# Kernel optimization log

Measured on AMD Instinct MI355X. Metric: run time of the kernel, lower is better.

The kernel has to match this reference:

```python
import jax, jax.numpy as jnp
import numpy as np

B, S, D, H, HD = 1, 4096, 1024, 16, 64
ROPE_THETA = 10000.0


def setup_inputs() -> dict:
    key = jax.random.key(0)
    ks = jax.random.split(key, 10)
    sc = 0.02
    hidden_states = jax.random.normal(ks[0], (B, S, D), dtype=jnp.float32)
    # sorted continuous timestamps in [0, S) (irregularly sampled time series)
    timestamps = jnp.sort(jax.random.uniform(ks[1], (B, S), dtype=jnp.float32), axis=-1) * S
    Wq = jax.random.normal(ks[2], (D, D), dtype=jnp.float32) * sc
    bq = jax.random.normal(ks[3], (D,), dtype=jnp.float32) * sc
    Wk = jax.random.normal(ks[4], (D, D), dtype=jnp.float32) * sc
    bk = jax.random.normal(ks[5], (D,), dtype=jnp.float32) * sc
    Wv = jax.random.normal(ks[6], (D, D), dtype=jnp.float32) * sc
    bv = jax.random.normal(ks[7], (D,), dtype=jnp.float32) * sc
    Wo = jax.random.normal(ks[8], (D, D), dtype=jnp.float32) * sc
    return dict(hidden_states=hidden_states, timestamps=timestamps,
                Wq=Wq, bq=bq, Wk=Wk, bk=bk, Wv=Wv, bv=bv, Wo=Wo)


def _rotate_half(x):
    x1, x2 = jnp.split(x, 2, axis=-1)
    return jnp.concatenate([-x2, x1], axis=-1)


def _ct_rope(q, k, timestamps):
    # q,k: [b,h,s,hd]; timestamps: [b,s] continuous positions
    inv_freq = 1.0 / (ROPE_THETA ** (jnp.arange(0, HD, 2, dtype=jnp.float32) / HD))
    angles = timestamps[:, None, :, None] * inv_freq  # [b,1,s,hd/2]
    angles = jnp.concatenate([angles, angles], axis=-1)  # [b,1,s,hd]
    cos, sin = jnp.cos(angles), jnp.sin(angles)
    q = q * cos + _rotate_half(q) * sin
    k = k * cos + _rotate_half(k) * sin
    return q, k


def reference(hidden_states, timestamps, Wq, bq, Wk, bk, Wv, bv, Wo):
    b, s, _ = hidden_states.shape
    # nn.Linear convention: y = x @ W.T + b
    q = (hidden_states @ Wq.T + bq).reshape(b, s, H, HD).transpose(0, 2, 1, 3)
    k = (hidden_states @ Wk.T + bk).reshape(b, s, H, HD).transpose(0, 2, 1, 3)
    v = (hidden_states @ Wv.T + bv).reshape(b, s, H, HD).transpose(0, 2, 1, 3)
    q, k = _ct_rope(q, k, timestamps)
    scores = jnp.einsum('bhqd,bhkd->bhqk', q, k) / jnp.sqrt(jnp.float32(HD))
    # causal additive mask (built as in HF Qwen2Model)
    causal = jnp.tril(jnp.ones((s, s), dtype=bool))
    neg = jnp.finfo(jnp.float32).min
    scores = jnp.where(causal[None, None], scores, neg)
    attn = jax.nn.softmax(scores.astype(jnp.float32), axis=-1).astype(q.dtype)
    out = jnp.einsum('bhqk,bhkd->bhqd', attn, v)
    out = out.transpose(0, 2, 1, 3).reshape(b, s, H * HD)
    return out @ Wo.T
```

## Files before the change

kernel.cpp:

```cpp
#include <hip/hip_runtime.h>

#define S_LEN  4096
#define DMODEL 1024
#define NHEAD  16
#define HDIM   64

typedef float    f32x4  __attribute__((ext_vector_type(4)));
typedef float    f32x16 __attribute__((ext_vector_type(16)));
typedef _Float16 f16x8  __attribute__((ext_vector_type(8)));
typedef _Float16 f16x4v __attribute__((ext_vector_type(4)));
typedef __fp16   fp16x2 __attribute__((ext_vector_type(2)));
typedef unsigned int u32;
typedef u32 u32x4 __attribute__((ext_vector_type(4)));

__device__ __forceinline__ void gl2lds16(const _Float16* g, _Float16* l) {
  __builtin_amdgcn_global_load_lds(
      (const __attribute__((address_space(1))) unsigned int*)g,
      (__attribute__((address_space(3))) unsigned int*)l, 16, 0, 0);
}

__device__ __forceinline__ u32 pkrtz_u(float a, float b) {
  fp16x2 h = __builtin_amdgcn_cvt_pkrtz(a, b);
  return __builtin_bit_cast(u32, h);
}

__device__ __forceinline__ float m3(float a, float b, float c) {
  return fmaxf(fmaxf(a, b), c);
}

__global__ void cast_f32_f16_k(const float* __restrict__ in,
                               _Float16* __restrict__ out, int n) {
  int i = (blockIdx.x * blockDim.x + threadIdx.x) * 4;
  if (i + 3 < n) {
    const float4 v = *(const float4*)(in + i);
    f16x4v o = { (_Float16)v.x, (_Float16)v.y, (_Float16)v.z, (_Float16)v.w };
    *(f16x4v*)(out + i) = o;
  }
}

__global__ void cast4_k(const float* __restrict__ a, const float* __restrict__ b,
                        const float* __restrict__ c, const float* __restrict__ d,
                        _Float16* __restrict__ oa, _Float16* __restrict__ ob,
                        _Float16* __restrict__ oc, _Float16* __restrict__ od) {
  const int seg = blockIdx.y;
  const float* in = seg == 0 ? a : seg == 1 ? b : seg == 2 ? c : d;
  _Float16*   out = seg == 0 ? oa : seg == 1 ? ob : seg == 2 ? oc : od;
  const int i = (blockIdx.x * blockDim.x + threadIdx.x) * 4;
  const float4 v = *(const float4*)(in + i);
  f16x4v o = { (_Float16)v.x, (_Float16)v.y, (_Float16)v.z, (_Float16)v.w };
  *(f16x4v*)(out + i) = o;
}

__global__ __launch_bounds__(256)
void gemm_qkv(const _Float16* __restrict__ A,
              const _Float16* __restrict__ Bw,
              const float* __restrict__ bq,
              const float* __restrict__ bk,
              const float* __restrict__ bv,
              const float* __restrict__ ts,
              _Float16* __restrict__ Qb,
              _Float16* __restrict__ Kb,
              _Float16* __restrict__ Vtb)
{
  __shared__ _Float16 lA[128 * 64];
  __shared__ _Float16 lB[128 * 64];

  const int tid  = threadIdx.x;
  const int wid  = tid >> 6;
  const int lane = tid & 63;
  const int l16  = lane & 15;
  const int lg   = lane >> 4;
  const int wr = wid >> 1, wc = wid & 1;
  const int m0 = blockIdx.y * 128, n0 = blockIdx.x * 128;
  const int K = DMODEL, M = S_LEN;

  const int lrow   = lane >> 3;
  const int gchunk = (lane & 7) ^ lrow;

  f32x4 acc[4][4] = {};

  for (int k0 = 0; k0 < K; k0 += 64) {
#pragma unroll
    for (int it = 0; it < 4; ++it) {
      const int rbase = (it * 4 + wid) * 8;
      gl2lds16(A  + (size_t)(m0 + rbase + lrow) * K + k0 + gchunk * 8, &lA[rbase * 64]);
      gl2lds16(Bw + (size_t)(n0 + rbase + lrow) * K + k0 + gchunk * 8, &lB[rbase * 64]);
    }
    __syncthreads();
#pragma unroll
    for (int kk = 0; kk < 2; ++kk) {
      f16x8 af[4], bfr[4];
#pragma unroll
      for (int mr = 0; mr < 4; ++mr) {
        const int row = wr * 64 + mr * 16 + l16;
        const int ch  = (kk * 4 + lg) ^ (l16 & 7);
        af[mr] = *(const f16x8*)&lA[row * 64 + ch * 8];
      }
#pragma unroll
      for (int nr = 0; nr < 4; ++nr) {
        const int row = wc * 64 + nr * 16 + l16;
        const int ch  = (kk * 4 + lg) ^ (l16 & 7);
        bfr[nr] = *(const f16x8*)&lB[row * 64 + ch * 8];
      }
#pragma unroll
      for (int mr = 0; mr < 4; ++mr)
#pragma unroll
        for (int nr = 0; nr < 4; ++nr)
          acc[mr][nr] = __builtin_amdgcn_mfma_f32_16x16x32_f16(af[mr], bfr[nr], acc[mr][nr], 0, 0, 0);
    }
    __syncthreads();
  }

  if (n0 >= 2048) {
    const int dbase = n0 - 2048;
    float bvv[4];
#pragma unroll
    for (int nr = 0; nr < 4; ++nr) bvv[nr] = bv[dbase + wc * 64 + nr * 16 + l16];
#pragma unroll
    for (int mr = 0; mr < 4; ++mr) {
      const int mbase = m0 + wr * 64 + mr * 16 + lg * 4;
#pragma unroll
      for (int nr = 0; nr < 4; ++nr) {
        const int d = dbase + wc * 64 + nr * 16 + l16;
        f16x4v o = { (_Float16)(acc[mr][nr][0] + bvv[nr]),
                     (_Float16)(acc[mr][nr][1] + bvv[nr]),
                     (_Float16)(acc[mr][nr][2] + bvv[nr]),
                     (_Float16)(acc[mr][nr][3] + bvv[nr]) };
        *(f16x4v*)&Vtb[(size_t)d * M + mbase] = o;
      }
    }
  } else {
    _Float16* O = (n0 < 1024) ? Qb : Kb;
    const float* bias = (n0 < 1024) ? bq : bk;
    const int nloc = n0 & 1023;
    float bvv[4];
#pragma unroll
    for (int nr = 0; nr < 4; ++nr) bvv[nr] = bias[nloc + wc * 64 + nr * 16 + l16];
    const float L2T  = 13.287712379549449f / 32.0f;
    const float inv0 = exp2f(-(float)l16 * L2T);
    const float inv1 = exp2f(-(float)(l16 + 16) * L2T);
#pragma unroll
    for (int mr = 0; mr < 4; ++mr)
#pragma unroll
      for (int r = 0; r < 4; ++r) {
        const int m = m0 + wr * 64 + mr * 16 + lg * 4 + r;
        const float t = ts[m];
        float s0, c0, s1, c1;
        sincosf(t * inv0, &s0, &c0);
        sincosf(t * inv1, &s1, &c1);
        const float p0 = acc[mr][0][r] + bvv[0];
        const float p1 = acc[mr][1][r] + bvv[1];
        const float p2 = acc[mr][2][r] + bvv[2];
        const float p3 = acc[mr][3][r] + bvv[3];
        const size_t base = (size_t)m * DMODEL + nloc + wc * 64 + l16;
        O[base + 0 ] = (_Float16)(p0 * c0 - p2 * s0);
        O[base + 16] = (_Float16)(p1 * c1 - p3 * s1);
        O[base + 32] = (_Float16)(p2 * c0 + p0 * s0);
        O[base + 48] = (_Float16)(p3 * c1 + p1 * s1);
      }
  }
}

__global__ __launch_bounds__(256)
void gemm_o(const _Float16* __restrict__ A,
            const _Float16* __restrict__ Bw,
            float* __restrict__ O)
{
  __shared__ _Float16 lA[128 * 64];
  __shared__ _Float16 lB[128 * 64];

  const int tid  = threadIdx.x;
  const int wid  = tid >> 6;
  const int lane = tid & 63;
  const int l16  = lane & 15;
  const int lg   = lane >> 4;
  const int wr = wid >> 1, wc = wid & 1;
  const int m0 = blockIdx.y * 128, n0 = blockIdx.x * 128;
  const int K = DMODEL, N = DMODEL;

  const int lrow   = lane >> 3;
  const int gchunk = (lane & 7) ^ lrow;

  f32x4 acc[4][4] = {};

  for (int k0 = 0; k0 < K; k0 += 64) {
#pragma unroll
    for (int it = 0; it < 4; ++it) {
      const int rbase = (it * 4 + wid) * 8;
      gl2lds16(A  + (size_t)(m0 + rbase + lrow) * K + k0 + gchunk * 8, &lA[rbase * 64]);
      gl2lds16(Bw + (size_t)(n0 + rbase + lrow) * K + k0 + gchunk * 8, &lB[rbase * 64]);
    }
    __syncthreads();
#pragma unroll
    for (int kk = 0; kk < 2; ++kk) {
      f16x8 af[4], bfr[4];
#pragma unroll
      for (int mr = 0; mr < 4; ++mr) {
        const int row = wr * 64 + mr * 16 + l16;
        const int ch  = (kk * 4 + lg) ^ (l16 & 7);
        af[mr] = *(const f16x8*)&lA[row * 64 + ch * 8];
      }
#pragma unroll
      for (int nr = 0; nr < 4; ++nr) {
        const int row = wc * 64 + nr * 16 + l16;
        const int ch  = (kk * 4 + lg) ^ (l16 & 7);
        bfr[nr] = *(const f16x8*)&lB[row * 64 + ch * 8];
      }
#pragma unroll
      for (int mr = 0; mr < 4; ++mr)
#pragma unroll
        for (int nr = 0; nr < 4; ++nr)
          acc[mr][nr] = __builtin_amdgcn_mfma_f32_16x16x32_f16(af[mr], bfr[nr], acc[mr][nr], 0, 0, 0);
    }
    __syncthreads();
  }

#pragma unroll
  for (int mr = 0; mr < 4; ++mr)
#pragma unroll
    for (int r = 0; r < 4; ++r) {
      const int m = m0 + wr * 64 + mr * 16 + lg * 4 + r;
#pragma unroll
      for (int nr = 0; nr < 4; ++nr) {
        const int n = n0 + wc * 64 + nr * 16 + l16;
        O[(size_t)m * N + n] = acc[mr][nr][r];
      }
    }
}

__device__ __forceinline__ void stage_tiles(const _Float16* __restrict__ Km,
                                            const _Float16* __restrict__ Vt,
                                            _Float16* kdst, _Float16* vdst,
                                            int kv0, int h, int wid, int lane) {
#pragma unroll
  for (int j8 = 0; j8 < 2; ++j8) {
    const int rb  = wid * 16 + j8 * 8;
    const int row = rb + (lane >> 3);
    const int g   = (lane & 7) ^ (row & 7);
    gl2lds16(Km + (size_t)(kv0 + row) * DMODEL + h * HDIM + g * 8, kdst + rb * 64);
    gl2lds16(Vt + (size_t)(h * HDIM + row) * S_LEN + kv0 + g * 8, vdst + rb * 64);
  }
}

__global__ __launch_bounds__(256, 4)
void attn_fwd(const _Float16* __restrict__ Q,
              const _Float16* __restrict__ Km,
              const _Float16* __restrict__ Vt,
              _Float16* __restrict__ Om,
              _Float16* __restrict__ pO,
              float* __restrict__ ps)
{
  __shared__ __align__(16) _Float16 smem[2][2][64 * 64];

  const int tid  = threadIdx.x;
  const int wid  = tid >> 6, lane = tid & 63;
  const int l31  = lane & 31;
  const bool hi  = (lane & 32) != 0;
  const int flat = blockIdx.x, xcd = flat & 7, idx = flat >> 3;
  const int h    = xcd * 2 + (idx & 1);
  const int slot = idx >> 1;
  int jb, part, parts;
  if (slot < 30)      { jb = 31 - slot / 3;            part = slot % 3;  parts = 3; }
  else if (slot < 52) { const int t2 = slot - 30; jb = 21 - (t2 >> 1); part = t2 & 1; parts = 2; }
  else                { jb = 62 - slot;                part = 0;        parts = 1; }
  const int nt  = 2 * jb + 2;
  const int kt0 = (nt * part) / parts, kt1 = (nt * (part + 1)) / parts;
  const bool partial = parts > 1;
  const int u = partial ? (h * 52 + ((jb <= 21) ? (jb - 11) * 2 : 22 + (jb - 22) * 3) + part) : 0;
  const int q0w = jb * 128 + wid * 32;
  const int sw  = l31 & 7;

  f16x8 qf[4];
  {
    const float qs = 0.18033688f;
    const size_t qbase = (size_t)(q0w + l31) * DMODEL + h * HDIM + (hi ? 8 : 0);
#pragma unroll
    for (int ks = 0; ks < 4; ++ks) {
      f16x8 t = *(const f16x8*)&Q[qbase + ks * 16];
#pragma unroll
      for (int e = 0; e < 8; ++e) qf[ks][e] = (_Float16)((float)t[e] * qs);
    }
  }

  f32x16 acc0, acc1;
#pragma unroll
  for (int r = 0; r < 16; ++r) { acc0[r] = 0.f; acc1[r] = 0.f; }
  float m_run = 0.f, l_run = 0.f;

  stage_tiles(Km, Vt, &smem[0][0][0], &smem[0][1][0], kt0 * 64, h, wid, lane);
  __syncthreads();
  int cur = 0;

  for (int kt = kt0; kt < kt1; ++kt) {
    if (kt + 1 < kt1)
      stage_tiles(Km, Vt, &smem[cur ^ 1][0][0], &smem[cur ^ 1][1][0],
                  (kt + 1) * 64, h, wid, lane);

    const int kv0 = kt * 64;
    if (kv0 <= q0w + 31) {
      const _Float16* kb = &smem[cur][0][0];
      const _Float16* vb = &smem[cur][1][0];

      f32x16 s0, s1;
#pragma unroll
      for (int r = 0; r < 16; ++r) { s0[r] = -m_run; s1[r] = -m_run; }
      __builtin_amdgcn_s_setprio(1);
#pragma unroll
      for (int ks = 0; ks < 4; ++ks) {
        const int cs = ((ks * 2 + (hi ? 1 : 0)) ^ sw) * 8;
        const f16x8 ka0 = *(const f16x8*)&kb[l31 * 64 + cs];
        const f16x8 ka1 = *(const f16x8*)&kb[(32 + l31) * 64 + cs];
        s0 = __builtin_amdgcn_mfma_f32_32x32x16_f16(ka0, qf[ks], s0, 0, 0, 0);
        s1 = __builtin_amdgcn_mfma_f32_32x32x16_f16(ka1, qf[ks], s1, 0, 0, 0);
      }
      __builtin_amdgcn_s_setprio(0);

      if (kv0 + 63 > q0w) {
        const int q = q0w + l31;
#pragma unroll
        for (int r = 0; r < 16; ++r) {
          const int kvr = kv0 + (r & 3) + 8 * (r >> 2) + (hi ? 4 : 0);
          if (kvr > q)      s0[r] = -1e30f;
          if (kvr + 32 > q) s1[r] = -1e30f;
        }
      }

      float t10[10];
#pragma unroll
      for (int p = 0; p < 5; ++p) {
        t10[p]     = m3(s0[3*p], s0[3*p+1], s0[3*p+2]);
        t10[5 + p] = m3(s1[3*p], s1[3*p+1], s1[3*p+2]);
      }
      float u0 = m3(t10[0], t10[1], t10[2]);
      float u1 = m3(t10[3], t10[4], s0[15]);
      float u2 = m3(t10[5], t10[6], t10[7]);
      float u3 = m3(t10[8], t10[9], s1[15]);
      float pm = fmaxf(m3(u0, u1, u2), u3);
      pm = fmaxf(pm, __shfl_xor(pm, 32));

      if (!__all(pm <= 10.f)) {
        m_run += pm;
        const float scl = exp2f(-pm);
        l_run *= scl;
#pragma unroll
        for (int r = 0; r < 16; ++r) { acc0[r] *= scl; acc1[r] *= scl; }
#pragma unroll
        for (int r = 0; r < 16; ++r) { s0[r] -= pm; s1[r] -= pm; }
      }

      float sa = 0.f, sb = 0.f, sc = 0.f, sd = 0.f;
#pragma unroll
      for (int r = 0; r < 16; r += 2) {
        s0[r]   = exp2f(s0[r]);
        s0[r+1] = exp2f(s0[r+1]);
        s1[r]   = exp2f(s1[r]);
        s1[r+1] = exp2f(s1[r+1]);
        sa += s0[r]; sb += s0[r+1]; sc += s1[r]; sd += s1[r+1];
      }
      float rsum = (sa + sb) + (sc + sd);
      rsum += __shfl_xor(rsum, 32);
      l_run += rsum;

      u32 pk[2][8];
#pragma unroll
      for (int p = 0; p < 8; ++p) {
        pk[0][p] = pkrtz_u(s0[2*p], s0[2*p+1]);
        pk[1][p] = pkrtz_u(s1[2*p], s1[2*p+1]);
      }

      __builtin_amdgcn_s_setprio(1);
#pragma unroll
      for (int ks = 0; ks < 4; ++ks) {
        const int c = ks >> 1, base = (ks & 1) * 4;
        auto r0 = __builtin_amdgcn_permlane32_swap((int)pk[c][base + 0], (int)pk[c][base + 2], false, false);
        auto r1 = __builtin_amdgcn_permlane32_swap((int)pk[c][base + 1], (int)pk[c][base + 3], false, false);
        u32x4 bw;
        bw[0] = (u32)r0[0];
        bw[1] = (u32)r1[0];
        bw[2] = (u32)r0[1];
        bw[3] = (u32)r1[1];
        const f16x8 pb = __builtin_bit_cast(f16x8, bw);
        const int cs = ((ks * 2 + (hi ? 1 : 0)) ^ sw) * 8;
        const f16x8 va0 = *(const f16x8*)&vb[l31 * 64 + cs];
        const f16x8 va1 = *(const f16x8*)&vb[(32 + l31) * 64 + cs];
        acc0 = __builtin_amdgcn_mfma_f32_32x32x16_f16(va0, pb, acc0, 0, 0, 0);
        acc1 = __builtin_amdgcn_mfma_f32_32x32x16_f16(va1, pb, acc1, 0, 0, 0);
      }
      __builtin_amdgcn_s_setprio(0);
    }

    __syncthreads();
    cur ^= 1;
  }

  _Float16* tr = &smem[0][0][0] + wid * 2304;
  const float invl = 1.0f / l_run;
#pragma unroll
  for (int r = 0; r < 16; ++r) {
    const int d = (r & 3) + 8 * (r >> 2) + (hi ? 4 : 0);
    tr[l31 * 72 + d]      = (_Float16)(acc0[r] * invl);
    tr[l31 * 72 + 32 + d] = (_Float16)(acc1[r] * invl);
  }
  __syncthreads();
  if (partial) {
    if (!hi) ps[u * 128 + wid * 32 + l31] = m_run + log2f(l_run);
    _Float16* dst = pO + (size_t)u * 8192;
#pragma unroll
    for (int cc = 0; cc < 4; ++cc) {
      const int qq = cc * 8 + (lane >> 3), c8 = lane & 7;
      const f16x8 v = *(const f16x8*)&tr[qq * 72 + c8 * 8];
      *(f16x8*)&dst[(wid * 32 + qq) * 64 + c8 * 8] = v;
    }
  } else {
#pragma unroll
    for (int cc = 0; cc < 4; ++cc) {
      const int qq = cc * 8 + (lane >> 3), c8 = lane & 7;
      const f16x8 v = *(const f16x8*)&tr[qq * 72 + c8 * 8];
      *(f16x8*)&Om[(size_t)(q0w + qq) * DMODEL + h * HDIM + c8 * 8] = v;
    }
  }
}

__global__ __launch_bounds__(256)
void combine_k(const _Float16* __restrict__ pO,
               const float* __restrict__ ps,
               _Float16* __restrict__ Om)
{
  const int t  = blockIdx.x * 256 + threadIdx.x;
  const int d8 = t & 7;
  const int hh = (t >> 3) & 15;
  const int q  = 1408 + (t >> 7);
  const int j  = q >> 7;
  const int qr = q & 127;
  const int parts = (j <= 21) ? 2 : 3;
  const int ul = (j <= 21) ? (j - 11) * 2 : 22 + (j - 22) * 3;
  const int u0 = hh * 52 + ul;

  float s[3];
  float S = -1e30f;
  for (int p = 0; p < parts; ++p) {
    s[p] = ps[(u0 + p) * 128 + qr];
    S = fmaxf(S, s[p]);
  }
  float o[8] = {0.f, 0.f, 0.f, 0.f, 0.f, 0.f, 0.f, 0.f};
  float tot = 0.f;
  for (int p = 0; p < parts; ++p) {
    const float w = exp2f(s[p] - S);
    tot += w;
    const f16x8 v = *(const f16x8*)&pO[(size_t)(u0 + p) * 8192 + qr * 64 + d8 * 8];
#pragma unroll
    for (int e = 0; e < 8; ++e) o[e] += w * (float)v[e];
  }
  const float inv = 1.0f / tot;
  f16x8 ov;
#pragma unroll
  for (int e = 0; e < 8; ++e) ov[e] = (_Float16)(o[e] * inv);
  *(f16x8*)&Om[(size_t)q * DMODEL + hh * 64 + d8 * 8] = ov;
}

extern "C" void kernel_launch(void* const* d_in, const int* in_sizes, int n_in,
                              void* d_out, int out_size, void* d_ws, size_t ws_size,
                              hipStream_t stream)
{
  const float* hs = (const float*)d_in[0];
  const float* ts = (const float*)d_in[1];
  const float* Wq = (const float*)d_in[2];
  const float* bq = (const float*)d_in[3];
  const float* Wk = (const float*)d_in[4];
  const float* bk = (const float*)d_in[5];
  const float* Wv = (const float*)d_in[6];
  const float* bv = (const float*)d_in[7];
  const float* Wo = (const float*)d_in[8];
  float* out = (float*)d_out;

  char* ws = (char*)d_ws;
  const size_t MB = 1024 * 1024;
  _Float16* hsb  = (_Float16*)(ws + 0 * MB);
  _Float16* wqb  = (_Float16*)(ws + 8 * MB);
  _Float16* wkb  = (_Float16*)(ws + 10 * MB);
  _Float16* wvb  = (_Float16*)(ws + 12 * MB);
  _Float16* wob  = (_Float16*)(ws + 14 * MB);
  _Float16* Qb   = (_Float16*)(ws + 16 * MB);
  _Float16* Kb   = (_Float16*)(ws + 24 * MB);
  _Float16* Vtb  = (_Float16*)(ws + 32 * MB);
  _Float16* attb = (_Float16*)(ws + 40 * MB);
  _Float16* pO   = (_Float16*)(ws + 0 * MB);
  float*    ps   = (float*)   (ws + (size_t)13631488);

  cast_f32_f16_k<<<dim3(4096), dim3(256), 0, stream>>>(hs, hsb, S_LEN * DMODEL);
  cast4_k<<<dim3(1024, 4), dim3(256), 0, stream>>>(Wq, Wk, Wv, Wo, wqb, wkb, wvb, wob);

  gemm_qkv<<<dim3(3072 / 128, S_LEN / 128), dim3(256), 0, stream>>>(
      hsb, wqb, bq, bk, bv, ts, Qb, Kb, Vtb);

  attn_fwd<<<dim3(1008), dim3(256), 0, stream>>>(Qb, Kb, Vtb, attb, pO, ps);
  combine_k<<<dim3(1344), dim3(256), 0, stream>>>(pO, ps, attb);

  gemm_o<<<dim3(DMODEL / 128, S_LEN / 128), dim3(256), 0, stream>>>(attb, wob, out);
}
```

Baseline: 162.3 us.

## Split long attention query blocks into up to five KV partitions and shrink gemm_o tile

Reworks the split-KV schedule for causal attention: query blocks are now split into 2–5 KV partitions depending on length (1440 blocks instead of 1008), and the combine kernel merges up to five partials. Partial outputs overflow into the output buffer as scratch, since it is only written by the final GEMM. The output projection GEMM tile height drops from 128 to 64 rows, doubling its grid. The intent is better load balance and CU occupancy on the long causal tail, at the cost of more partial-write and combine traffic.

```diff
diff --git a/kernel.cpp b/kernel.cpp
--- a/kernel.cpp
+++ b/kernel.cpp
@@ -166,7 +166,7 @@
             const _Float16* __restrict__ Bw,
             float* __restrict__ O)
 {
-  __shared__ _Float16 lA[128 * 64];
+  __shared__ _Float16 lA[64 * 64];
   __shared__ _Float16 lB[128 * 64];
 
   const int tid  = threadIdx.x;
@@ -175,28 +175,32 @@
   const int l16  = lane & 15;
   const int lg   = lane >> 4;
   const int wr = wid >> 1, wc = wid & 1;
-  const int m0 = blockIdx.y * 128, n0 = blockIdx.x * 128;
+  const int m0 = blockIdx.y * 64, n0 = blockIdx.x * 128;
   const int K = DMODEL, N = DMODEL;
 
   const int lrow   = lane >> 3;
   const int gchunk = (lane & 7) ^ lrow;
 
-  f32x4 acc[4][4] = {};
+  f32x4 acc[2][4] = {};
 
   for (int k0 = 0; k0 < K; k0 += 64) {
+#pragma unroll
+    for (int it = 0; it < 2; ++it) {
+      const int rbase = (it * 4 + wid) * 8;
+      gl2lds16(A + (size_t)(m0 + rbase + lrow) * K + k0 + gchunk * 8, &lA[rbase * 64]);
+    }
 #pragma unroll
     for (int it = 0; it < 4; ++it) {
       const int rbase = (it * 4 + wid) * 8;
-      gl2lds16(A  + (size_t)(m0 + rbase + lrow) * K + k0 + gchunk * 8, &lA[rbase * 64]);
       gl2lds16(Bw + (size_t)(n0 + rbase + lrow) * K + k0 + gchunk * 8, &lB[rbase * 64]);
     }
     __syncthreads();
 #pragma unroll
     for (int kk = 0; kk < 2; ++kk) {
-      f16x8 af[4], bfr[4];
-#pragma unroll
-      for (int mr = 0; mr < 4; ++mr) {
-        const int row = wr * 64 + mr * 16 + l16;
+      f16x8 af[2], bfr[4];
+#pragma unroll
+      for (int mr = 0; mr < 2; ++mr) {
+        const int row = wr * 32 + mr * 16 + l16;
         const int ch  = (kk * 4 + lg) ^ (l16 & 7);
         af[mr] = *(const f16x8*)&lA[row * 64 + ch * 8];
       }
@@ -207,7 +211,7 @@
         bfr[nr] = *(const f16x8*)&lB[row * 64 + ch * 8];
       }
 #pragma unroll
-      for (int mr = 0; mr < 4; ++mr)
+      for (int mr = 0; mr < 2; ++mr)
 #pragma unroll
         for (int nr = 0; nr < 4; ++nr)
           acc[mr][nr] = __builtin_amdgcn_mfma_f32_16x16x32_f16(af[mr], bfr[nr], acc[mr][nr], 0, 0, 0);
@@ -216,10 +220,10 @@
   }
 
 #pragma unroll
-  for (int mr = 0; mr < 4; ++mr)
+  for (int mr = 0; mr < 2; ++mr)
 #pragma unroll
     for (int r = 0; r < 4; ++r) {
-      const int m = m0 + wr * 64 + mr * 16 + lg * 4 + r;
+      const int m = m0 + wr * 32 + mr * 16 + lg * 4 + r;
 #pragma unroll
       for (int nr = 0; nr < 4; ++nr) {
         const int n = n0 + wc * 64 + nr * 16 + l16;
@@ -242,12 +246,20 @@
   }
 }
 
+__device__ __forceinline__ int part_off(int jb) {
+  if (jb >= 28) return 63 + (jb - 28) * 5;
+  if (jb >= 21) return 35 + (jb - 21) * 4;
+  if (jb >= 14) return 14 + (jb - 14) * 3;
+  return (jb - 7) * 2;
+}
+
 __global__ __launch_bounds__(256, 4)
 void attn_fwd(const _Float16* __restrict__ Q,
               const _Float16* __restrict__ Km,
               const _Float16* __restrict__ Vt,
               _Float16* __restrict__ Om,
-              _Float16* __restrict__ pO,
+              _Float16* __restrict__ pO0,
+              _Float16* __restrict__ pO1,
               float* __restrict__ ps)
 {
   __shared__ __align__(16) _Float16 smem[2][2][64 * 64];
@@ -260,13 +272,15 @@
   const int h    = xcd * 2 + (idx & 1);
   const int slot = idx >> 1;
   int jb, part, parts;
-  if (slot < 30)      { jb = 31 - slot / 3;            part = slot % 3;  parts = 3; }
-  else if (slot < 52) { const int t2 = slot - 30; jb = 21 - (t2 >> 1); part = t2 & 1; parts = 2; }
-  else                { jb = 62 - slot;                part = 0;        parts = 1; }
+  if (slot < 20)      { jb = 31 - slot / 5;                 part = slot % 5;  parts = 5; }
+  else if (slot < 48) { const int t = slot - 20; jb = 27 - t / 4; part = t % 4; parts = 4; }
+  else if (slot < 69) { const int t = slot - 48; jb = 20 - t / 3; part = t % 3; parts = 3; }
+  else if (slot < 83) { const int t = slot - 69; jb = 13 - t / 2; part = t % 2; parts = 2; }
+  else                { jb = 89 - slot;                     part = 0;        parts = 1; }
   const int nt  = 2 * jb + 2;
   const int kt0 = (nt * part) / parts, kt1 = (nt * (part + 1)) / parts;
   const bool partial = parts > 1;
-  const int u = partial ? (h * 52 + ((jb <= 21) ? (jb - 11) * 2 : 22 + (jb - 22) * 3) + part) : 0;
+  const int u = partial ? (h * 83 + part_off(jb) + part) : 0;
   const int q0w = jb * 128 + wid * 32;
   const int sw  = l31 & 7;
 
@@ -404,7 +418,8 @@
   __syncthreads();
   if (partial) {
     if (!hi) ps[u * 128 + wid * 32 + l31] = m_run + log2f(l_run);
-    _Float16* dst = pO + (size_t)u * 8192;
+    _Float16* dst = (u < 832) ? (pO0 + (size_t)u * 8192)
+                              : (pO1 + (size_t)(u - 832) * 8192);
 #pragma unroll
     for (int cc = 0; cc < 4; ++cc) {
       const int qq = cc * 8 + (lane >> 3), c8 = lane & 7;
@@ -422,34 +437,44 @@
 }
 
 __global__ __launch_bounds__(256)
-void combine_k(const _Float16* __restrict__ pO,
+void combine_k(const _Float16* __restrict__ pO0,
+               const _Float16* __restrict__ pO1,
                const float* __restrict__ ps,
                _Float16* __restrict__ Om)
 {
   const int t  = blockIdx.x * 256 + threadIdx.x;
   const int d8 = t & 7;
   const int hh = (t >> 3) & 15;
-  const int q  = 1408 + (t >> 7);
+  const int q  = 896 + (t >> 7);
   const int j  = q >> 7;
   const int qr = q & 127;
-  const int parts = (j <= 21) ? 2 : 3;
-  const int ul = (j <= 21) ? (j - 11) * 2 : 22 + (j - 22) * 3;
-  const int u0 = hh * 52 + ul;
-
-  float s[3];
-  float S = -1e30f;
-  for (int p = 0; p < parts; ++p) {
-    s[p] = ps[(u0 + p) * 128 + qr];
-    S = fmaxf(S, s[p]);
-  }
+  const int parts = (j >= 28) ? 5 : (j >= 21) ? 4 : (j >= 14) ? 3 : 2;
+  const int off   = (j >= 28) ? 63 + (j - 28) * 5
+                  : (j >= 21) ? 35 + (j - 21) * 4
+                  : (j >= 14) ? 14 + (j - 14) * 3
+                  :             (j - 7) * 2;
+  const int u0 = hh * 83 + off;
+
+  float sv[5];
+#pragma unroll
+  for (int p = 0; p < 5; ++p)
+    sv[p] = (p < parts) ? ps[(u0 + p) * 128 + qr] : -1e30f;
+  const float S = fmaxf(m3(sv[0], sv[1], sv[2]), fmaxf(sv[3], sv[4]));
+
   float o[8] = {0.f, 0.f, 0.f, 0.f, 0.f, 0.f, 0.f, 0.f};
   float tot = 0.f;
-  for (int p = 0; p < parts; ++p) {
-    const float w = exp2f(s[p] - S);
-    tot += w;
-    const f16x8 v = *(const f16x8*)&pO[(size_t)(u0 + p) * 8192 + qr * 64 + d8 * 8];
-#pragma unroll
-    for (int e = 0; e < 8; ++e) o[e] += w * (float)v[e];
+#pragma unroll
+  for (int p = 0; p < 5; ++p) {
+    if (p < parts) {
+      const float w = exp2f(sv[p] - S);
+      tot += w;
+      const int uu = u0 + p;
+      const _Float16* pp = (uu < 832) ? (pO0 + (size_t)uu * 8192)
+                                      : (pO1 + (size_t)(uu - 832) * 8192);
+      const f16x8 v = *(const f16x8*)&pp[qr * 64 + d8 * 8];
+#pragma unroll
+      for (int e = 0; e < 8; ++e) o[e] += w * (float)v[e];
+    }
   }
   const float inv = 1.0f / tot;
   f16x8 ov;
@@ -484,7 +509,8 @@
   _Float16* Kb   = (_Float16*)(ws + 24 * MB);
   _Float16* Vtb  = (_Float16*)(ws + 32 * MB);
   _Float16* attb = (_Float16*)(ws + 40 * MB);
-  _Float16* pO   = (_Float16*)(ws + 0 * MB);
+  _Float16* pO0  = (_Float16*)(ws + 0 * MB);
+  _Float16* pO1  = (_Float16*)d_out;
   float*    ps   = (float*)   (ws + (size_t)13631488);
 
   cast_f32_f16_k<<<dim3(4096), dim3(256), 0, stream>>>(hs, hsb, S_LEN * DMODEL);
@@ -493,8 +519,8 @@
   gemm_qkv<<<dim3(3072 / 128, S_LEN / 128), dim3(256), 0, stream>>>(
       hsb, wqb, bq, bk, bv, ts, Qb, Kb, Vtb);
 
-  attn_fwd<<<dim3(1008), dim3(256), 0, stream>>>(Qb, Kb, Vtb, attb, pO, ps);
-  combine_k<<<dim3(1344), dim3(256), 0, stream>>>(pO, ps, attb);
-
-  gemm_o<<<dim3(DMODEL / 128, S_LEN / 128), dim3(256), 0, stream>>>(attb, wob, out);
-}
+  attn_fwd<<<dim3(1440), dim3(256), 0, stream>>>(Qb, Kb, Vtb, attb, pO0, pO1, ps);
+  combine_k<<<dim3(1600), dim3(256), 0, stream>>>(pO0, pO1, ps, attb);
+
+  gemm_o<<<dim3(DMODEL / 128, S_LEN / 64), dim3(256), 0, stream>>>(attb, wob, out);
+}
```

After: 154.7 us. 1.05x faster.
